# Kernel tuning notes

Measured on AMD Instinct MI355X. Metric: run time of the kernel, lower is better.

## Reference

```python
import jax, jax.numpy as jnp
import numpy as np

B, N, NPOINT, NSAMPLE = 16, 4096, 1024, 32
RADIUS = 0.2
CHANNELS = [6, 64, 64, 128]
EPS = 1e-5


def farthest_point_sample(xyz, npoint):
    # xyz: [B,N,3] -> idx [B,npoint]; deterministic start at index 0
    b, n, _ = xyz.shape
    def step(carry, _):
        dist, far = carry
        centroid = jnp.take_along_axis(xyz, far[:, None, None], axis=1)  # [B,1,3]
        d = jnp.sum((xyz - centroid) ** 2, axis=-1)  # [B,N]
        dist = jnp.minimum(dist, d)
        return (dist, jnp.argmax(dist, axis=-1).astype(jnp.int32)), far
    init = (jnp.full((b, n), 1e10, dtype=xyz.dtype), jnp.zeros((b,), jnp.int32))
    _, cents = jax.lax.scan(step, init, None, length=npoint)
    return cents.T  # [B,npoint]


def query_ball_point(radius, nsample, xyz, new_xyz):
    # xyz [B,N,3], new_xyz [B,S,3] -> idx [B,S,nsample]
    b, n, _ = xyz.shape
    d2 = (jnp.sum(new_xyz ** 2, -1)[:, :, None]
          + jnp.sum(xyz ** 2, -1)[:, None, :]
          - 2.0 * jnp.einsum('bsc,bnc->bsn', new_xyz, xyz))  # [B,S,N]
    cand = jnp.where(d2 > radius * radius, n, jnp.arange(n, dtype=jnp.int32)[None, None, :])
    # smallest nsample candidate indices (== torch sort[:, :, :nsample])
    neg_top, _ = jax.lax.top_k(-cand, nsample)
    idx = -neg_top  # ascending smallest indices
    first = idx[:, :, 0:1]
    return jnp.where(idx == n, first, idx)


def gather_points(pts, idx):
    # pts [B,N,C], idx [B,S,K] -> [B,S,K,C]
    b, s, k = idx.shape
    flat = idx.reshape(b, s * k)
    out = jnp.take_along_axis(pts, flat[:, :, None], axis=1)
    return out.reshape(b, s, k, pts.shape[-1])


def _forward(xyz, points, params):
    fps_idx = farthest_point_sample(xyz, NPOINT)  # [B,S]
    new_xyz = jnp.take_along_axis(xyz, fps_idx[:, :, None], axis=1)  # [B,S,3]
    idx = query_ball_point(RADIUS, NSAMPLE, xyz, new_xyz)  # [B,S,K]
    grouped_xyz = gather_points(xyz, idx) - new_xyz[:, :, None, :]  # [B,S,K,3]
    grouped_pts = gather_points(points, idx)  # [B,S,K,D]
    x = jnp.concatenate([grouped_xyz, grouped_pts], axis=-1)  # [B,S,K,6]
    for (W, g, bta, m, v) in params:
        x = jnp.einsum('bskc,cd->bskd', x, W)
        x = (x - m) * (g * jax.lax.rsqrt(v + EPS)) + bta  # BN (inference stats)
        x = jax.nn.relu(x)
    feat = jnp.max(x, axis=2)  # [B,S,Cout]
    return new_xyz, feat


def setup_inputs() -> dict:
    key = jax.random.key(0)
    ks = jax.random.split(key, 16)
    xyz = jax.random.uniform(ks[0], (B, N, 3), dtype=jnp.float32)
    points = jax.random.normal(ks[1], (B, N, 3), dtype=jnp.float32)
    inp = {'xyz': xyz, 'points': points}
    ki = 2
    for li in range(3):
        cin, cout = CHANNELS[li], CHANNELS[li + 1]
        inp[f'W{li+1}'] = jax.random.normal(ks[ki], (cin, cout), dtype=jnp.float32) * (1.0 / np.sqrt(cin)); ki += 1
        inp[f'g{li+1}'] = jnp.ones((cout,), jnp.float32)
        inp[f'b{li+1}'] = jnp.zeros((cout,), jnp.float32)
        inp[f'm{li+1}'] = jax.random.normal(ks[ki], (cout,), dtype=jnp.float32) * 0.1; ki += 1
        inp[f'v{li+1}'] = jax.random.uniform(ks[ki], (cout,), dtype=jnp.float32, minval=0.5, maxval=1.5); ki += 1
    return inp


def reference(xyz, points, W1, g1, b1, m1, v1, W2, g2, b2, m2, v2, W3, g3, b3, m3, v3):
    params = [(W1, g1, b1, m1, v1), (W2, g2, b2, m2, v2), (W3, g3, b3, m3, v3)]
    return _forward(xyz, points, params)
```

## Files before the change

kernel.cpp:

```cpp
#include <hip/hip_runtime.h>

#define BATCH   16
#define NPTS    4096
#define NPOINT  1024
#define NSAMPLE 32

__global__ __launch_bounds__(256, 1)
void fps_kernel(const float* __restrict__ xyz, float* __restrict__ new_xyz)
{
    const int b    = blockIdx.x;
    const int t    = threadIdx.x;
    const int lane = t & 63;
    const int wv   = t >> 6;
    const float* xb = xyz + (size_t)b * NPTS * 3;

    __shared__ float sxyz[NPTS * 3];
    __shared__ __align__(16) unsigned long long sCand[2][4];

    float px[16], py[16], pz[16], dist[16];
#pragma unroll
    for (int j = 0; j < 16; ++j) {
        const int n = j * 256 + t;
        float X = xb[n * 3 + 0];
        float Y = xb[n * 3 + 1];
        float Z = xb[n * 3 + 2];
        sxyz[n * 3 + 0] = X; sxyz[n * 3 + 1] = Y; sxyz[n * 3 + 2] = Z;
        asm volatile("" : "+v"(X), "+v"(Y), "+v"(Z));
        px[j] = X; py[j] = Y; pz[j] = Z; dist[j] = 1e10f;
    }
    __syncthreads();

    float cx = sxyz[0], cy = sxyz[1], cz = sxyz[2];
    float* out = new_xyz + (size_t)b * NPOINT * 3;

    for (int i = 0; i < NPOINT; ++i) {
        if (t == 0) { out[i*3+0] = cx; out[i*3+1] = cy; out[i*3+2] = cz; }

        float bval = -1.0f; int bidx = 0;
#pragma unroll
        for (int j = 0; j < 16; ++j) {
            float dx = __fsub_rn(px[j], cx);
            float dy = __fsub_rn(py[j], cy);
            float dz = __fsub_rn(pz[j], cz);
            float d  = __fadd_rn(__fadd_rn(__fmul_rn(dx, dx), __fmul_rn(dy, dy)),
                                 __fmul_rn(dz, dz));
            float nd = fminf(dist[j], d);
            dist[j] = nd;
            if (nd > bval) { bval = nd; bidx = j * 256 + t; }
        }

        unsigned long long cand =
            ((unsigned long long)__float_as_uint(bval) << 32) |
            (unsigned long long)(unsigned int)~bidx;

#define DPP_RED(CTRL, RMASK)                                                   \
        {                                                                      \
            unsigned int oh = (unsigned int)__builtin_amdgcn_update_dpp(       \
                0, (int)(unsigned int)(cand >> 32), (CTRL), (RMASK), 0xF, true);\
            unsigned int ol = (unsigned int)__builtin_amdgcn_update_dpp(       \
                0, (int)(unsigned int)cand, (CTRL), (RMASK), 0xF, true);       \
            unsigned long long o =                                             \
                ((unsigned long long)oh << 32) | (unsigned long long)ol;       \
            if (o > cand) cand = o;                                            \
        }
        DPP_RED(0x121, 0xF)
        DPP_RED(0x122, 0xF)
        DPP_RED(0x124, 0xF)
        DPP_RED(0x128, 0xF)
        DPP_RED(0x142, 0xA)
        DPP_RED(0x143, 0xC)
#undef DPP_RED

        const int par = i & 1;
        if (lane == 63) sCand[par][wv] = cand;
        __syncthreads();

        const ulonglong2* pc = (const ulonglong2*)&sCand[par][0];
        ulonglong2 r0 = pc[0], r1 = pc[1];
        unsigned long long m01 = (r0.y > r0.x) ? r0.y : r0.x;
        unsigned long long m23 = (r1.y > r1.x) ? r1.y : r1.x;
        unsigned long long m   = (m23 > m01) ? m23 : m01;
        const unsigned int ix = ~(unsigned int)m;

        cx = sxyz[ix * 3 + 0];
        cy = sxyz[ix * 3 + 1];
        cz = sxyz[ix * 3 + 2];
    }
}

__global__ __launch_bounds__(256)
void ball_kernel(const float* __restrict__ xyz, const float* __restrict__ new_xyz,
                 int* __restrict__ idx)
{
    const int q    = blockIdx.x * 4 + (threadIdx.x >> 6);
    const int lane = threadIdx.x & 63;
    const int b    = q >> 10;
    const float* xb = xyz + (size_t)b * NPTS * 3;

    const float s0 = new_xyz[q*3+0];
    const float s1 = new_xyz[q*3+1];
    const float s2 = new_xyz[q*3+2];
    const float ssum = __fadd_rn(__fadd_rn(__fmul_rn(s0,s0), __fmul_rn(s1,s1)),
                                 __fmul_rn(s2,s2));
    const float r2 = (float)(0.2 * 0.2);

    int* myidx = idx + (size_t)q * NSAMPLE;
    int found = 0;
    int first = -1;

    for (int c = 0; c < NPTS / 64 && found < NSAMPLE; ++c) {
        int n = c * 64 + lane;
        float x = xb[n*3+0], y = xb[n*3+1], z = xb[n*3+2];
        float nsum = __fadd_rn(__fadd_rn(__fmul_rn(x,x), __fmul_rn(y,y)), __fmul_rn(z,z));
        float dot  = __fmaf_rn(s2, z, __fmaf_rn(s1, y, __fmul_rn(s0, x)));
        float d2   = __fsub_rn(__fadd_rn(ssum, nsum), __fmul_rn(2.0f, dot));
        bool inb = !(d2 > r2);
        unsigned long long m = __ballot(inb);
        if (first < 0 && m != 0ull) first = c * 64 + (int)__builtin_ctzll(m);
        if (inb) {
            int rank = __popcll(m & ((1ull << lane) - 1ull));
            int slot = found + rank;
            if (slot < NSAMPLE) myidx[slot] = n;
        }
        found += __popcll(m);
    }
    if (found > NSAMPLE) found = NSAMPLE;
    for (int slot = found + lane; slot < NSAMPLE; slot += 64) myidx[slot] = first;
}

__global__ __launch_bounds__(256)
void mlp_kernel(const float* __restrict__ xyz, const float* __restrict__ points,
                const float* __restrict__ new_xyz, const int* __restrict__ idx,
                const float* __restrict__ W1, const float* __restrict__ g1,
                const float* __restrict__ b1, const float* __restrict__ m1,
                const float* __restrict__ v1,
                const float* __restrict__ W2, const float* __restrict__ g2,
                const float* __restrict__ b2, const float* __restrict__ m2,
                const float* __restrict__ v2,
                const float* __restrict__ W3, const float* __restrict__ g3,
                const float* __restrict__ b3, const float* __restrict__ m3,
                const float* __restrict__ v3,
                float* __restrict__ feat)
{
    __shared__ float w1t[64][8];
    __shared__ float w2t[64][64];
    __shared__ float w3t[128][64];
    __shared__ float bias1s[64], bias2s[64], bias3s[128];
    __shared__ float sc1[64], sc2[64], sc3[128];

    const int tid = threadIdx.x;

    for (int d = tid; d < 64; d += 256) {
        float s1v = g1[d] / sqrtf(v1[d] + 1e-5f);
        sc1[d] = s1v; bias1s[d] = b1[d] - m1[d] * s1v;
        float s2v = g2[d] / sqrtf(v2[d] + 1e-5f);
        sc2[d] = s2v; bias2s[d] = b2[d] - m2[d] * s2v;
    }
    for (int d = tid; d < 128; d += 256) {
        float s3v = g3[d] / sqrtf(v3[d] + 1e-5f);
        sc3[d] = s3v; bias3s[d] = b3[d] - m3[d] * s3v;
    }
    __syncthreads();
    for (int e = tid; e < 64 * 8; e += 256) {
        int d = e >> 3, c = e & 7;
        w1t[d][c] = (c < 6) ? W1[c * 64 + d] * sc1[d] : 0.f;
    }
    for (int e = tid; e < 64 * 64; e += 256) {
        int d = e >> 6, c = e & 63;
        w2t[d][c] = W2[c * 64 + d] * sc2[d];
    }
    for (int e = tid; e < 128 * 64; e += 256) {
        int d = e >> 6, c = e & 63;
        w3t[d][c] = W3[c * 128 + d] * sc3[d];
    }
    __syncthreads();

    const int wid  = tid >> 6;
    const int lane = tid & 63;
    const int q = blockIdx.x * 8 + wid * 2 + (lane >> 5);
    const int k = lane & 31;
    const int b = q >> 10;

    const int n = idx[(size_t)q * NSAMPLE + k];
    const float* xp = xyz    + ((size_t)b * NPTS + n) * 3;
    const float* pp = points + ((size_t)b * NPTS + n) * 3;
    const float* nx = new_xyz + (size_t)q * 3;

    const float in0 = __fsub_rn(xp[0], nx[0]);
    const float in1 = __fsub_rn(xp[1], nx[1]);
    const float in2 = __fsub_rn(xp[2], nx[2]);
    const float in3 = pp[0], in4 = pp[1], in5 = pp[2];

    float x1[64];
#pragma unroll
    for (int d = 0; d < 64; ++d) {
        const float4 wa = *(const float4*)&w1t[d][0];
        const float4 wb = *(const float4*)&w1t[d][4];
        float acc = bias1s[d];
        acc = fmaf(in0, wa.x, acc);
        acc = fmaf(in1, wa.y, acc);
        acc = fmaf(in2, wa.z, acc);
        acc = fmaf(in3, wa.w, acc);
        acc = fmaf(in4, wb.x, acc);
        acc = fmaf(in5, wb.y, acc);
        x1[d] = fmaxf(acc, 0.f);
    }

    float x2[64];
#pragma unroll
    for (int d = 0; d < 64; ++d) {
        float acc = bias2s[d];
        const float4* wr = (const float4*)w2t[d];
#pragma unroll
        for (int cc = 0; cc < 16; ++cc) {
            float4 w = wr[cc];
            acc = fmaf(x1[4*cc+0], w.x, acc);
            acc = fmaf(x1[4*cc+1], w.y, acc);
            acc = fmaf(x1[4*cc+2], w.z, acc);
            acc = fmaf(x1[4*cc+3], w.w, acc);
        }
        x2[d] = fmaxf(acc, 0.f);
    }

    float* fq = feat + (size_t)q * 128;
    for (int d = 0; d < 128; ++d) {
        float acc = bias3s[d];
        const float4* wr = (const float4*)w3t[d];
#pragma unroll
        for (int cc = 0; cc < 16; ++cc) {
            float4 w = wr[cc];
            acc = fmaf(x2[4*cc+0], w.x, acc);
            acc = fmaf(x2[4*cc+1], w.y, acc);
            acc = fmaf(x2[4*cc+2], w.z, acc);
            acc = fmaf(x2[4*cc+3], w.w, acc);
        }
        float vv = fmaxf(acc, 0.f);
#pragma unroll
        for (int off = 16; off >= 1; off >>= 1)
            vv = fmaxf(vv, __shfl_xor(vv, off));
        if (k == 0) fq[d] = vv;
    }
}

extern "C" void kernel_launch(void* const* d_in, const int* in_sizes, int n_in,
                              void* d_out, int out_size, void* d_ws, size_t ws_size,
                              hipStream_t stream)
{
    (void)in_sizes; (void)n_in; (void)out_size; (void)ws_size;

    const float* xyz    = (const float*)d_in[0];
    const float* points = (const float*)d_in[1];
    const float* W1 = (const float*)d_in[2];
    const float* g1 = (const float*)d_in[3];
    const float* b1 = (const float*)d_in[4];
    const float* m1 = (const float*)d_in[5];
    const float* v1 = (const float*)d_in[6];
    const float* W2 = (const float*)d_in[7];
    const float* g2 = (const float*)d_in[8];
    const float* b2 = (const float*)d_in[9];
    const float* m2 = (const float*)d_in[10];
    const float* v2 = (const float*)d_in[11];
    const float* W3 = (const float*)d_in[12];
    const float* g3 = (const float*)d_in[13];
    const float* b3 = (const float*)d_in[14];
    const float* m3 = (const float*)d_in[15];
    const float* v3 = (const float*)d_in[16];

    float* out_f    = (float*)d_out;
    float* new_xyz  = out_f;
    float* feat     = out_f + (size_t)BATCH * NPOINT * 3;
    int*   idx      = (int*)d_ws;

    fps_kernel <<<BATCH, 256, 0, stream>>>(xyz, new_xyz);
    ball_kernel<<<(BATCH * NPOINT) / 4, 256, 0, stream>>>(xyz, new_xyz, idx);
    mlp_kernel <<<(BATCH * NPOINT) / 8, 256, 0, stream>>>(xyz, points, new_xyz, idx,
        W1, g1, b1, m1, v1, W2, g2, b2, m2, v2, W3, g3, b3, m3, v3, feat);
}
```

Measured before the change: 945.0 us.

## Widen FPS kernel to 1024 threads with DPP cross-wave reduction

Result: slower. 1.142 ms (+20.8%).

```diff
diff --git a/kernel.cpp b/kernel.cpp
--- a/kernel.cpp
+++ b/kernel.cpp
@@ -5,7 +5,7 @@
 #define NPOINT  1024
 #define NSAMPLE 32
 
-__global__ __launch_bounds__(256, 1)
+__global__ __launch_bounds__(1024)
 void fps_kernel(const float* __restrict__ xyz, float* __restrict__ new_xyz)
 {
     const int b    = blockIdx.x;
@@ -15,12 +15,12 @@
     const float* xb = xyz + (size_t)b * NPTS * 3;
 
     __shared__ float sxyz[NPTS * 3];
-    __shared__ __align__(16) unsigned long long sCand[2][4];
-
-    float px[16], py[16], pz[16], dist[16];
-#pragma unroll
-    for (int j = 0; j < 16; ++j) {
-        const int n = j * 256 + t;
+    __shared__ __align__(16) unsigned long long sCand[2][16];
+
+    float px[4], py[4], pz[4], dist[4];
+#pragma unroll
+    for (int j = 0; j < 4; ++j) {
+        const int n = j * 1024 + t;
         float X = xb[n * 3 + 0];
         float Y = xb[n * 3 + 1];
         float Z = xb[n * 3 + 2];
@@ -38,7 +38,7 @@
 
         float bval = -1.0f; int bidx = 0;
 #pragma unroll
-        for (int j = 0; j < 16; ++j) {
+        for (int j = 0; j < 4; ++j) {
             float dx = __fsub_rn(px[j], cx);
             float dy = __fsub_rn(py[j], cy);
             float dz = __fsub_rn(pz[j], cz);
@@ -46,41 +46,41 @@
                                  __fmul_rn(dz, dz));
             float nd = fminf(dist[j], d);
             dist[j] = nd;
-            if (nd > bval) { bval = nd; bidx = j * 256 + t; }
+            if (nd > bval) { bval = nd; bidx = j * 1024 + t; }
         }
 
         unsigned long long cand =
             ((unsigned long long)__float_as_uint(bval) << 32) |
             (unsigned long long)(unsigned int)~bidx;
 
-#define DPP_RED(CTRL, RMASK)                                                   \
+#define DPP_RED(VAR, CTRL, RMASK)                                              \
         {                                                                      \
             unsigned int oh = (unsigned int)__builtin_amdgcn_update_dpp(       \
-                0, (int)(unsigned int)(cand >> 32), (CTRL), (RMASK), 0xF, true);\
+                0, (int)(unsigned int)(VAR >> 32), (CTRL), (RMASK), 0xF, true);\
             unsigned int ol = (unsigned int)__builtin_amdgcn_update_dpp(       \
-                0, (int)(unsigned int)cand, (CTRL), (RMASK), 0xF, true);       \
+                0, (int)(unsigned int)VAR, (CTRL), (RMASK), 0xF, true);        \
             unsigned long long o =                                             \
                 ((unsigned long long)oh << 32) | (unsigned long long)ol;       \
-            if (o > cand) cand = o;                                            \
-        }
-        DPP_RED(0x121, 0xF)
-        DPP_RED(0x122, 0xF)
-        DPP_RED(0x124, 0xF)
-        DPP_RED(0x128, 0xF)
-        DPP_RED(0x142, 0xA)
-        DPP_RED(0x143, 0xC)
-#undef DPP_RED
+            if (o > VAR) VAR = o;                                              \
+        }
+        DPP_RED(cand, 0x121, 0xF)
+        DPP_RED(cand, 0x122, 0xF)
+        DPP_RED(cand, 0x124, 0xF)
+        DPP_RED(cand, 0x128, 0xF)
+        DPP_RED(cand, 0x142, 0xA)
+        DPP_RED(cand, 0x143, 0xC)
 
         const int par = i & 1;
         if (lane == 63) sCand[par][wv] = cand;
         __syncthreads();
 
-        const ulonglong2* pc = (const ulonglong2*)&sCand[par][0];
-        ulonglong2 r0 = pc[0], r1 = pc[1];
-        unsigned long long m01 = (r0.y > r0.x) ? r0.y : r0.x;
-        unsigned long long m23 = (r1.y > r1.x) ? r1.y : r1.x;
-        unsigned long long m   = (m23 > m01) ? m23 : m01;
-        const unsigned int ix = ~(unsigned int)m;
+        unsigned long long c2 = sCand[par][lane & 15];
+        DPP_RED(c2, 0x121, 0xF)
+        DPP_RED(c2, 0x122, 0xF)
+        DPP_RED(c2, 0x124, 0xF)
+        DPP_RED(c2, 0x128, 0xF)
+#undef DPP_RED
+        const unsigned int ix = ~(unsigned int)c2;
 
         cx = sxyz[ix * 3 + 0];
         cy = sxyz[ix * 3 + 1];
@@ -271,7 +271,7 @@
     float* feat     = out_f + (size_t)BATCH * NPOINT * 3;
     int*   idx      = (int*)d_ws;
 
-    fps_kernel <<<BATCH, 256, 0, stream>>>(xyz, new_xyz);
+    fps_kernel <<<BATCH, 1024, 0, stream>>>(xyz, new_xyz);
     ball_kernel<<<(BATCH * NPOINT) / 4, 256, 0, stream>>>(xyz, new_xyz, idx);
     mlp_kernel <<<(BATCH * NPOINT) / 8, 256, 0, stream>>>(xyz, points, new_xyz, idx,
         W1, g1, b1, m1, v1, W2, g2, b2, m2, v2, W3, g3, b3, m3, v3, feat);
```
